# Optimization experiments

Hardware: AMD Instinct MI355X
Metric: run time of the kernel (lower is better)

## Reference

```python
import jax, jax.numpy as jnp
import numpy as np

SCALE_BASE = 512
EPS = 1e-5


def _xpos_factors(seq_len, head_dim):
    half = head_dim // 2
    # xpos scale vector: ((arange(0, hd, 2) + 0.4*hd) / (1.4*hd)) ** (pos / scale_base)
    s = (jnp.arange(0, head_dim, 2, dtype=jnp.float32) + 0.4 * head_dim) / (1.4 * head_dim)
    pos = jnp.arange(seq_len, dtype=jnp.float32)
    scale = s[None, :] ** (pos[:, None] / SCALE_BASE)          # (S, half)
    inv_freq = 1.0 / (10000.0 ** (jnp.arange(half, dtype=jnp.float32) / half))
    ang = pos[:, None] * inv_freq[None, :]                     # (S, half)
    return jnp.sin(ang), jnp.cos(ang), scale


def _dup_interleave(m):
    # (S, half) -> (S, head_dim): each column duplicated, interleaved
    return jnp.repeat(m, 2, axis=-1)


def _rotate_every_two(x):
    x1, x2 = x[..., ::2], x[..., 1::2]
    return jnp.stack((-x2, x1), axis=-1).reshape(x.shape)


def _apply_xpos(x, sin, cos, scale):
    sinf = _dup_interleave(sin * scale)                        # (S, hd)
    cosf = _dup_interleave(cos * scale)
    return x * cosf + _rotate_every_two(x) * sinf


def _decay_mask(gammas, seq_len, chunk_size):
    # D[h, i, j] = gamma_h ** |i - j| if j < ((i // chunk) + 1) * chunk else 0
    i = jnp.arange(seq_len)[:, None]
    j = jnp.arange(seq_len)[None, :]
    allowed = j < ((i // chunk_size) + 1) * chunk_size         # (S, S)
    expo = jnp.abs(i - j).astype(jnp.float32)
    D = gammas[:, None, None] ** expo[None]                    # (H, S, S)
    return jnp.where(allowed[None], D, 0.0)


def setup_inputs() -> dict:
    key = jax.random.key(0)
    B, S, hidden, H, hd, chunk = 4, 2048, 512, 8, 64, 64
    ks = jax.random.split(key, 6)
    return {
        "X": jax.random.normal(ks[0], (B, S, hidden), dtype=jnp.float32),
        "W_Q": jax.random.normal(ks[1], (H, hidden, hd), dtype=jnp.float32) / hidden,
        "W_K": jax.random.normal(ks[2], (H, hidden, hd), dtype=jnp.float32) / hidden,
        "W_V": jax.random.normal(ks[3], (H, hidden, hd), dtype=jnp.float32) / hidden,
        "W_G": jax.random.normal(ks[4], (hidden, H * hd), dtype=jnp.float32) / hidden,
        "W_O": jax.random.normal(ks[5], (H * hd, hidden), dtype=jnp.float32) / hidden,
        "gn_weight": jnp.ones((H * hd,), dtype=jnp.float32),
        "gn_bias": jnp.zeros((H * hd,), dtype=jnp.float32),
        "chunk_size": chunk,
    }


def reference(X, W_Q, W_K, W_V, W_G, W_O, gn_weight, gn_bias, chunk_size):
    B, S, hidden = X.shape
    H, _, hd = W_Q.shape
    # RetNet multi-scale decay rates
    gammas = 1.0 - jnp.exp(
        jnp.linspace(jnp.log(jnp.float32(1 / 32)), jnp.log(jnp.float32(1 / 512)), H)
    )
    D = _decay_mask(gammas, S, chunk_size)                     # (H, S, S)

    # per-head projections: n = heads
    Q = jnp.einsum("bsh,nhd->bnsd", X, W_Q)
    K = jnp.einsum("bsh,nhd->bnsd", X, W_K)
    V = jnp.einsum("bsh,nhd->bnsd", X, W_V)

    sin, cos, scale = _xpos_factors(S, hd)
    Q = _apply_xpos(Q, sin, cos, scale)                        # broadcast (S,hd) over (B,H,S,hd)
    K = _apply_xpos(K, sin, cos, 1.0 / scale)                  # downscale

    scores = jnp.einsum("bnsd,bntd->bnst", Q, K) * D[None]     # (B,H,S,S)
    Yh = jnp.einsum("bnst,bntd->bnsd", scores, V)              # (B,H,S,hd)

    # concat heads -> (B,S,H*hd), GroupNorm(heads) per token (stats over each head's hd channels)
    Y = Yh.transpose(0, 2, 1, 3)                               # (B,S,H,hd)
    mu = Y.mean(-1, keepdims=True)
    var = Y.var(-1, keepdims=True)
    Yn = (Y - mu) / jnp.sqrt(var + EPS)
    Yn = Yn.reshape(B, S, H * hd) * gn_weight + gn_bias

    gate = jax.nn.silu(X @ W_G)                                # swish(X W_G)
    return (gate * Yn) @ W_O
```

## Files before the change

kernel.cpp:

```cpp
#include <hip/hip_runtime.h>

#define B_   4
#define S_   2048
#define HID  512
#define H_   8
#define HD   64

typedef __attribute__((ext_vector_type(8))) short bf16x8;
typedef __attribute__((ext_vector_type(4))) float f32x4;

#define MFMA16(a, b, c) __builtin_amdgcn_mfma_f32_16x16x32_bf16(a, b, c, 0, 0, 0)

#define GAMMA_L0   (-3.4657359027997265f)
#define GAMMA_STEP (-0.3960841031771116f)

__device__ __forceinline__ void async16(const void* g, void* l) {
    __builtin_amdgcn_global_load_lds(
        (const __attribute__((address_space(1))) void*)g,
        (__attribute__((address_space(3))) void*)l, 16, 0, 0);
}

__device__ __forceinline__ unsigned short f2bf(float x) {
    unsigned u = __float_as_uint(x);
    return (unsigned short)((u + 0x7fffu + ((u >> 16) & 1u)) >> 16);
}
__device__ __forceinline__ float bfs2f(short s) {
    return __uint_as_float(((unsigned)(unsigned short)s) << 16);
}
__device__ __forceinline__ unsigned packbf(float lo, float hi) {
    return (unsigned)f2bf(lo) | ((unsigned)f2bf(hi) << 16);
}

__global__ __launch_bounds__(256) void prep(
    const float* __restrict__ X,
    const float* __restrict__ Wq, const float* __restrict__ Wk,
    const float* __restrict__ Wv, const float* __restrict__ Wg,
    const float* __restrict__ Wo,
    short* __restrict__ Xb,
    short* __restrict__ WqT, short* __restrict__ WkT, short* __restrict__ WvT,
    short* __restrict__ WgT, short* __restrict__ WoT,
    float4* __restrict__ Lut)
{
    __shared__ float T[64][65];
    const int bid = blockIdx.x, t = threadIdx.x;

    if (bid < 2048) {
        size_t i = ((size_t)bid * 256 + t) * 8;
        float4 a = *(const float4*)&X[i];
        float4 b = *(const float4*)&X[i + 4];
        union { int4 v; unsigned short s[8]; } u;
        u.s[0] = f2bf(a.x); u.s[1] = f2bf(a.y); u.s[2] = f2bf(a.z); u.s[3] = f2bf(a.w);
        u.s[4] = f2bf(b.x); u.s[5] = f2bf(b.y); u.s[6] = f2bf(b.z); u.s[7] = f2bf(b.w);
        *(int4*)&Xb[i] = u.v;
        return;
    }
    if (bid >= 2368) {
        int idx = (bid - 2368) * 256 + t;
        int s = idx >> 5, k = idx & 31;
        float invf = exp2f(-0.41524101186092035f * (float)k);
        float ang  = (float)s * invf;
        float sn = sinf(ang), cs = cosf(ang);
        float sk = ((float)(2 * k) + 25.6f) / 89.6f;
        float sc = exp2f(log2f(sk) * (float)s * (1.0f / 512.0f));
        Lut[idx] = (float4){cs * sc, sn * sc, cs / sc, sn / sc};
        return;
    }

    const int wb = bid - 2048;
    const float* ip; short* op; int ild;
    if (wb < 192) {
        int which = wb >> 6, rem = wb & 63, h = rem >> 3, kt = rem & 7;
        const float* src = which == 0 ? Wq : which == 1 ? Wk : Wv;
        short* dst       = which == 0 ? WqT : which == 1 ? WkT : WvT;
        ip = src + ((size_t)h * 512 + kt * 64) * 64;
        ild = 64;
        op = dst + (size_t)(h * 64) * 512 + kt * 64;
    } else {
        int rem = wb - 192, which = rem >> 6, r3 = rem & 63, nt = r3 >> 3, kt = r3 & 7;
        const float* src = which ? Wo : Wg;
        short* dst       = which ? WoT : WgT;
        ip = src + (size_t)(kt * 64) * 512 + nt * 64;
        ild = 512;
        op = dst + (size_t)(nt * 64) * 512 + kt * 64;
    }
    {
        int r = t >> 2, c0 = (t & 3) * 16;
        #pragma unroll
        for (int e = 0; e < 4; ++e) {
            float4 f = *(const float4*)&ip[(size_t)r * ild + c0 + e * 4];
            T[r][c0 + e*4 + 0] = f.x; T[r][c0 + e*4 + 1] = f.y;
            T[r][c0 + e*4 + 2] = f.z; T[r][c0 + e*4 + 3] = f.w;
        }
    }
    __syncthreads();
    {
        int cc = t >> 2, r0 = (t & 3) * 16;
        short* orow = op + (size_t)cc * 512;
        #pragma unroll
        for (int ii = 0; ii < 8; ++ii) {
            int lo = f2bf(T[r0 + 2*ii][cc]);
            int hi = f2bf(T[r0 + 2*ii + 1][cc]);
            *(int*)(orow + r0 + 2*ii) = (lo & 0xffff) | (hi << 16);
        }
    }
}

__device__ __forceinline__ void gemm_core64(const short* __restrict__ Ag,
                                            const short* __restrict__ Bg,
                                            short* As, short* Bs,
                                            f32x4 (&acc)[2][4])
{
    const int tid = threadIdx.x;
    const int L = tid & 63, quad = L >> 4, l16 = L & 15;
    const int w = tid >> 6;
    const int wrow = (w >> 1) * 32, wcol = (w & 1) * 64;

    for (int k0 = 0; k0 < 512; k0 += 32) {
        {
            int row = tid >> 2, c4 = (tid & 3) ^ (row & 3);
            async16(Ag + (size_t)row * 512 + k0 + c4 * 8, As + tid * 8);
        }
        #pragma unroll
        for (int j = 0; j < 2; ++j) {
            int idx = j * 256 + tid;
            int row = idx >> 2, c4 = (idx & 3) ^ (row & 3);
            async16(Bg + (size_t)row * 512 + k0 + c4 * 8, Bs + idx * 8);
        }
        __syncthreads();

        bf16x8 af[2], bfr[4];
        #pragma unroll
        for (int a = 0; a < 2; ++a) {
            int m = wrow + a * 16 + l16;
            af[a] = *(const bf16x8*)&As[m * 32 + (quad ^ (m & 3)) * 8];
        }
        #pragma unroll
        for (int b = 0; b < 4; ++b) {
            int n = wcol + b * 16 + l16;
            bfr[b] = *(const bf16x8*)&Bs[n * 32 + (quad ^ (n & 3)) * 8];
        }
        #pragma unroll
        for (int a = 0; a < 2; ++a)
            #pragma unroll
            for (int b = 0; b < 4; ++b)
                acc[a][b] = MFMA16(af[a], bfr[b], acc[a][b]);
        __syncthreads();
    }
}

__global__ __launch_bounds__(256) void fused_gemm(
    const short* __restrict__ Xb, const short* __restrict__ WT,
    const float4* __restrict__ Lut,
    short* __restrict__ Qb, short* __restrict__ Kb, short* __restrict__ Vb,
    short* __restrict__ Gb)
{
    __shared__ short SM[64 * 136];
    f32x4 acc[2][4];
    #pragma unroll
    for (int a = 0; a < 2; ++a)
        #pragma unroll
        for (int b = 0; b < 4; ++b) acc[a][b] = (f32x4){0.f, 0.f, 0.f, 0.f};

    gemm_core64(Xb + (size_t)blockIdx.y * 64 * 512,
                WT + (size_t)blockIdx.x * 128 * 512, SM, SM + 2048, acc);

    const int tid = threadIdx.x, L = tid & 63, quad = L >> 4, l16 = L & 15;
    const int w = tid >> 6, wrow = (w >> 1) * 32, wcol = (w & 1) * 64;
    const int zone = blockIdx.x >> 2;
    short* Out = (zone == 0) ? Qb : (zone == 1) ? Kb : Vb;

    #pragma unroll
    for (int b = 0; b < 4; ++b) {
        int ncol = (blockIdx.x & 3) * 128 + wcol + b * 16 + l16;
        int d = ncol & 63, k = d >> 1;
        int colE = wcol + b * 16 + (l16 & ~1);
        #pragma unroll
        for (int a = 0; a < 2; ++a) {
            #pragma unroll
            for (int r = 0; r < 4; ++r) {
                int m = blockIdx.y * 64 + wrow + a * 16 + quad * 4 + r;
                int s = m & 2047;
                float v = acc[a][b][r];
                unsigned word;
                if (zone == 3) {
                    float g = v / (1.0f + __expf(-v));
                    float part = __shfl_xor(g, 1);
                    word = packbf(g, part);
                } else {
                    float part = __shfl_xor(v, 1);
                    float e = (d & 1) ? part : v;
                    float o = (d & 1) ? v : part;
                    if (zone == 2) {
                        word = packbf(e, o);
                    } else {
                        float4 f = Lut[s * 32 + k];
                        float cs = (zone == 0) ? f.x : f.z;
                        float sn = (zone == 0) ? f.y : f.w;
                        word = packbf(e * cs - o * sn, o * cs + e * sn);
                    }
                }
                if (!(l16 & 1))
                    *(int*)&SM[(wrow + a * 16 + quad * 4 + r) * 136 + colE] = word;
            }
        }
    }
    __syncthreads();
    #pragma unroll
    for (int j = 0; j < 4; ++j) {
        int idx = j * 256 + tid;
        int row = idx >> 4, c0 = (idx & 15) * 8;
        int m = blockIdx.y * 64 + row;
        int n = (blockIdx.x & 3) * 128 + c0;
        if (zone == 3) {
            *(int4*)&Gb[(size_t)m * 512 + n] = *(const int4*)&SM[row * 136 + c0];
        } else {
            int bb = m >> 11, s = m & 2047;
            int h = n >> 6, d = n & 63;
            *(int4*)&Out[(((size_t)bb * 8 + h) * 2048 + s) * 64 + d] =
                *(const int4*)&SM[row * 136 + c0];
        }
    }
}

__global__ __launch_bounds__(256) void out_gemm(
    const short* __restrict__ Zb, const short* __restrict__ WoT,
    float* __restrict__ Of)
{
    __shared__ short SM[6144];
    f32x4 acc[2][4];
    #pragma unroll
    for (int a = 0; a < 2; ++a)
        #pragma unroll
        for (int b = 0; b < 4; ++b) acc[a][b] = (f32x4){0.f, 0.f, 0.f, 0.f};

    gemm_core64(Zb + (size_t)blockIdx.y * 64 * 512,
                WoT + (size_t)blockIdx.x * 128 * 512, SM, SM + 2048, acc);

    const int tid = threadIdx.x, L = tid & 63, quad = L >> 4, l16 = L & 15;
    const int w = tid >> 6, wrow = (w >> 1) * 32, wcol = (w & 1) * 64;
    #pragma unroll
    for (int b = 0; b < 4; ++b) {
        int ncol = blockIdx.x * 128 + wcol + b * 16 + l16;
        #pragma unroll
        for (int a = 0; a < 2; ++a)
            #pragma unroll
            for (int r = 0; r < 4; ++r) {
                int m = blockIdx.y * 64 + wrow + a * 16 + quad * 4 + r;
                Of[(size_t)m * 512 + ncol] = acc[a][b][r];
            }
    }
}

__global__ __launch_bounds__(256) void ret_g(
    const short* __restrict__ Kb, const short* __restrict__ Vb,
    short* __restrict__ Gt)
{
    __shared__ short Kt[64 * 72];
    __shared__ short Vt[64 * 72];
    const int tid = threadIdx.x, L = tid & 63, quad = L >> 4, l16 = L & 15;
    const int w = tid >> 6;
    const int c = blockIdx.x, bn = blockIdx.y, hh = bn & 7;

    float gamma = 1.0f - expf(GAMMA_L0 + GAMMA_STEP * (float)hh);
    float lg = log2f(gamma);

    {
        const short* kg = Kb + ((size_t)bn * 2048 + c * 64 + L) * 64 + w * 16;
        const short* vg = Vb + ((size_t)bn * 2048 + c * 64 + L) * 64 + w * 16;
        float wgt = exp2f(lg * (float)(64 - L));
        int4 k0 = *(const int4*)kg; int4 k1 = *(const int4*)(kg + 8);
        int4 v0 = *(const int4*)vg; int4 v1 = *(const int4*)(vg + 8);
        short* kt = Kt + L; short* vt = Vt + L;
        #pragma unroll
        for (int q = 0; q < 4; ++q) {
            int uk = ((const int*)&k0)[q];
            kt[(w*16 + 2*q)     * 72] = (short)f2bf(bfs2f((short)uk) * wgt);
            kt[(w*16 + 2*q + 1) * 72] = (short)f2bf(bfs2f((short)(uk >> 16)) * wgt);
            int uv = ((const int*)&v0)[q];
            vt[(w*16 + 2*q)     * 72] = (short)uv;
            vt[(w*16 + 2*q + 1) * 72] = (short)(uv >> 16);
        }
        #pragma unroll
        for (int q = 0; q < 4; ++q) {
            int uk = ((const int*)&k1)[q];
            kt[(w*16 + 8 + 2*q) * 72] = (short)f2bf(bfs2f((short)uk) * wgt);
            kt[(w*16 + 9 + 2*q) * 72] = (short)f2bf(bfs2f((short)(uk >> 16)) * wgt);
            int uv = ((const int*)&v1)[q];
            vt[(w*16 + 8 + 2*q) * 72] = (short)uv;
            vt[(w*16 + 9 + 2*q) * 72] = (short)(uv >> 16);
        }
    }
    __syncthreads();

    bf16x8 a0 = *(const bf16x8*)&Vt[(w * 16 + l16) * 72 + quad * 8];
    bf16x8 a1 = *(const bf16x8*)&Vt[(w * 16 + l16) * 72 + 32 + quad * 8];
    short* Gp = Gt + ((size_t)bn * 32 + c) * 4096;
    #pragma unroll
    for (int b = 0; b < 4; ++b) {
        bf16x8 b0 = *(const bf16x8*)&Kt[(b * 16 + l16) * 72 + quad * 8];
        bf16x8 b1 = *(const bf16x8*)&Kt[(b * 16 + l16) * 72 + 32 + quad * 8];
        f32x4 acc = (f32x4){0.f, 0.f, 0.f, 0.f};
        acc = MFMA16(a0, b0, acc);
        acc = MFMA16(a1, b1, acc);
        #pragma unroll
        for (int r = 0; r < 4; ++r) {
            float v = acc[r];
            float part = __shfl_xor(v, 1);
            unsigned word = packbf(v, part);
            if (!(l16 & 1))
                *(int*)&Gp[(w*16 + quad*4 + r) * 64 + b * 16 + (l16 & ~1)] = word;
        }
    }
}

__global__ __launch_bounds__(256) void ret_scan(short* __restrict__ GM)
{
    const int tid = threadIdx.x, seg = blockIdx.x, bn = blockIdx.y, hh = bn & 7;
    float gamma = 1.0f - expf(GAMMA_L0 + GAMMA_STEP * (float)hh);
    float g64 = exp2f(log2f(gamma) * 64.0f);

    size_t base = (size_t)bn * 32 * 4096 + seg * 1024 + tid * 4;
    float m0 = 0.f, m1 = 0.f, m2 = 0.f, m3 = 0.f;
    #pragma unroll 4
    for (int c = 0; c < 32; ++c) {
        int2* p = (int2*)&GM[base + (size_t)c * 4096];
        int2 g = *p;
        *p = make_int2((int)packbf(m0, m1), (int)packbf(m2, m3));
        m0 = g64 * m0 + bfs2f((short)g.x);
        m1 = g64 * m1 + bfs2f((short)(g.x >> 16));
        m2 = g64 * m2 + bfs2f((short)g.y);
        m3 = g64 * m3 + bfs2f((short)(g.y >> 16));
    }
}

__global__ __launch_bounds__(256) void ret_main(
    const short* __restrict__ Qb, const short* __restrict__ Kb,
    const short* __restrict__ Vb, const short* __restrict__ Mb,
    short* __restrict__ Yb)
{
    __shared__ short Qs[4096];
    __shared__ short Ks[4096];
    __shared__ short Ms[4096];
    __shared__ short Vt[64 * 72];
    __shared__ short Pw[4][16 * 72];

    const int tid = threadIdx.x, L = tid & 63, quad = L >> 4, l16 = L & 15;
    const int w = tid >> 6;
    const int c = blockIdx.x, bn = blockIdx.y, hh = bn & 7, bb = bn >> 3;

    float gamma = 1.0f - expf(GAMMA_L0 + GAMMA_STEP * (float)hh);
    float lg = log2f(gamma);

    float Dabs[4][4];
    #pragma unroll
    for (int b = 0; b < 4; ++b)
        #pragma unroll
        for (int r = 0; r < 4; ++r) {
            int dlt = (w * 16 + quad * 4 + r) - (b * 16 + l16);
            Dabs[b][r] = exp2f(lg * fabsf((float)dlt));
        }
    float gq[4];
    #pragma unroll
    for (int r = 0; r < 4; ++r)
        gq[r] = exp2f(lg * (float)(w * 16 + quad * 4 + r));

    {
        const short* qg = Qb + ((size_t)bn * 2048 + c * 64 + w * 16 + (L >> 2)) * 64 + (L & 3) * 8;
        async16(qg,      Qs + w * 512 + L * 8);
        async16(qg + 32, Qs + 2048 + w * 512 + L * 8);
        const short* kg = Kb + ((size_t)bn * 2048 + c * 64 + w * 16 + (L >> 2)) * 64 + (L & 3) * 8;
        async16(kg,      Ks + w * 512 + L * 8);
        async16(kg + 32, Ks + 2048 + w * 512 + L * 8);
        const short* mg = Mb + ((size_t)bn * 32 + c) * 4096 + (w * 16 + (L >> 2)) * 64 + (L & 3) * 8;
        async16(mg,      Ms + w * 512 + L * 8);
        async16(mg + 32, Ms + 2048 + w * 512 + L * 8);
    }
    {
        const short* vg = Vb + ((size_t)bn * 2048 + c * 64 + L) * 64 + w * 16;
        int4 v0 = *(const int4*)vg;
        int4 v1 = *(const int4*)(vg + 8);
        short* vt = Vt + L;
        #pragma unroll
        for (int q = 0; q < 4; ++q) {
            int u = ((const int*)&v0)[q];
            vt[(w*16 + 2*q)     * 72] = (short)u;
            vt[(w*16 + 2*q + 1) * 72] = (short)(u >> 16);
        }
        #pragma unroll
        for (int q = 0; q < 4; ++q) {
            int u = ((const int*)&v1)[q];
            vt[(w*16 + 8 + 2*q) * 72] = (short)u;
            vt[(w*16 + 9 + 2*q) * 72] = (short)(u >> 16);
        }
    }
    __syncthreads();

    bf16x8 aQ0 = *(const bf16x8*)&Qs[(w * 16 + l16) * 32 + quad * 8];
    bf16x8 aQ1 = *(const bf16x8*)&Qs[2048 + (w * 16 + l16) * 32 + quad * 8];
    f32x4 accM[4];
    #pragma unroll
    for (int b = 0; b < 4; ++b) {
        bf16x8 k0 = *(const bf16x8*)&Ks[(b * 16 + l16) * 32 + quad * 8];
        bf16x8 k1 = *(const bf16x8*)&Ks[2048 + (b * 16 + l16) * 32 + quad * 8];
        f32x4 S = (f32x4){0.f, 0.f, 0.f, 0.f};
        S = MFMA16(aQ0, k0, S);
        S = MFMA16(aQ1, k1, S);
        #pragma unroll
        for (int r = 0; r < 4; ++r)
            Pw[w][(quad * 4 + r) * 72 + b * 16 + l16] = (short)f2bf(S[r] * Dabs[b][r]);

        bf16x8 m0 = *(const bf16x8*)&Ms[(b * 16 + l16) * 32 + quad * 8];
        bf16x8 m1 = *(const bf16x8*)&Ms[2048 + (b * 16 + l16) * 32 + quad * 8];
        f32x4 Mv = (f32x4){0.f, 0.f, 0.f, 0.f};
        Mv = MFMA16(aQ0, m0, Mv);
        Mv = MFMA16(aQ1, m1, Mv);
        accM[b] = Mv;
    }

    bf16x8 aP0 = *(const bf16x8*)&Pw[w][l16 * 72 + quad * 8];
    bf16x8 aP1 = *(const bf16x8*)&Pw[w][l16 * 72 + 32 + quad * 8];
    #pragma unroll
    for (int b2 = 0; b2 < 4; ++b2) {
        bf16x8 v0f = *(const bf16x8*)&Vt[(b2 * 16 + l16) * 72 + quad * 8];
        bf16x8 v1f = *(const bf16x8*)&Vt[(b2 * 16 + l16) * 72 + 32 + quad * 8];
        f32x4 y = accM[b2];
        f32x4 yv = (f32x4){0.f, 0.f, 0.f, 0.f};
        yv = MFMA16(aP0, v0f, yv);
        yv = MFMA16(aP1, v1f, yv);
        #pragma unroll
        for (int r = 0; r < 4; ++r) {
            float yy = yv[r] + gq[r] * y[r];
            float part = __shfl_xor(yy, 1);
            unsigned word = packbf(yy, part);
            if (!(l16 & 1)) {
                int il = w * 16 + quad * 4 + r;
                int d = b2 * 16 + (l16 & ~1);
                *(int*)&Yb[(((size_t)bb * 2048 + c * 64 + il) * 8 + hh) * 64 + d] = word;
            }
        }
    }
}

__global__ __launch_bounds__(256) void gn_kernel(
    const short* __restrict__ Yb, const short* __restrict__ Gb,
    const float* __restrict__ gw, const float* __restrict__ gb,
    short* __restrict__ Zb)
{
    const int t = threadIdx.x, w = t >> 6, L = t & 63;
    const int unit = blockIdx.x * 4 + w;
    const size_t idx = (size_t)unit * 64 + L;

    float y = bfs2f(Yb[idx]);
    float sum = y, sq = y * y;
    #pragma unroll
    for (int off = 32; off; off >>= 1) {
        sum += __shfl_xor(sum, off);
        sq  += __shfl_xor(sq, off);
    }
    float mu  = sum * (1.0f / 64.0f);
    float var = sq * (1.0f / 64.0f) - mu * mu;
    float rstd = rsqrtf(var + 1e-5f);

    int j = (unit & 7) * 64 + L;
    float yn = (y - mu) * rstd * gw[j] + gb[j];
    Zb[idx] = (short)f2bf(bfs2f(Gb[idx]) * yn);
}

extern "C" void kernel_launch(void* const* d_in, const int* in_sizes, int n_in,
                              void* d_out, int out_size, void* d_ws, size_t ws_size,
                              hipStream_t stream)
{
    const float* X  = (const float*)d_in[0];
    const float* Wq = (const float*)d_in[1];
    const float* Wk = (const float*)d_in[2];
    const float* Wv = (const float*)d_in[3];
    const float* Wg = (const float*)d_in[4];
    const float* Wo = (const float*)d_in[5];
    const float* gw = (const float*)d_in[6];
    const float* gb = (const float*)d_in[7];

    char* ws = (char*)d_ws;
    short* Xb  = (short*)ws;
    short* WqT = (short*)(ws + 8388608);
    short* WkT = WqT + 262144;
    short* WvT = WkT + 262144;
    short* WgT = WvT + 262144;
    short* WoT = WgT + 262144;
    short* Qb  = (short*)(ws + 11010048);
    short* Kb  = Qb + 4194304;
    short* Vb  = Kb + 4194304;
    float4* Lut = (float4*)(ws + 36175872);
    short* GM  = (short*)(ws + 37224448);
    short* Yb  = (short*)(ws + 45613056);
    short* Gb  = (short*)(ws + 54001664);
    short* Zb  = Vb;

    prep<<<2624, 256, 0, stream>>>(X, Wq, Wk, Wv, Wg, Wo,
                                   Xb, WqT, WkT, WvT, WgT, WoT, Lut);
    fused_gemm<<<dim3(16, 128), 256, 0, stream>>>(Xb, WqT, Lut, Qb, Kb, Vb, Gb);
    ret_g<<<dim3(32, 32), 256, 0, stream>>>(Kb, Vb, GM);
    ret_scan<<<dim3(4, 32), 256, 0, stream>>>(GM);
    ret_main<<<dim3(32, 32), 256, 0, stream>>>(Qb, Kb, Vb, GM, Yb);
    gn_kernel<<<16384, 256, 0, stream>>>(Yb, Gb, gw, gb, Zb);
    out_gemm<<<dim3(4, 128), 256, 0, stream>>>(Zb, WoT, (float*)d_out);
}
```

Baseline: 183.9 us.

## Double-buffer GEMM K loop and fuse GroupNorm+gate into retention kernel

The shared GEMM core now double-buffers its LDS tiles so the async load of the next K slice overlaps the MFMAs on the current one, with one barrier per iteration and a changed XOR swizzle. GroupNorm statistics, affine transform and the silu-gate multiply move into the epilogue of ret_main using in-wave shuffles, which removes the gn_kernel launch and the round trip of Y through global memory. Costs are twice the LDS per GEMM block, which may lower occupancy, and a heavier ret_main epilogue with scattered Gb reads.

```diff
diff --git a/kernel.cpp b/kernel.cpp
--- a/kernel.cpp
+++ b/kernel.cpp
@@ -105,47 +105,60 @@
     }
 }
 
+__device__ __forceinline__ void stage64(const short* __restrict__ Ag,
+                                        const short* __restrict__ Bg,
+                                        int k0, short* As, short* Bs, int tid)
+{
+    {
+        int row = tid >> 2, c4 = (tid & 3) ^ ((row >> 1) & 3);
+        async16(Ag + (size_t)row * 512 + k0 + c4 * 8, As + tid * 8);
+    }
+    #pragma unroll
+    for (int j = 0; j < 2; ++j) {
+        int idx = j * 256 + tid;
+        int row = idx >> 2, c4 = (idx & 3) ^ ((row >> 1) & 3);
+        async16(Bg + (size_t)row * 512 + k0 + c4 * 8, Bs + idx * 8);
+    }
+}
+
 __device__ __forceinline__ void gemm_core64(const short* __restrict__ Ag,
                                             const short* __restrict__ Bg,
-                                            short* As, short* Bs,
-                                            f32x4 (&acc)[2][4])
+                                            short* SM, f32x4 (&acc)[2][4])
 {
     const int tid = threadIdx.x;
     const int L = tid & 63, quad = L >> 4, l16 = L & 15;
     const int w = tid >> 6;
     const int wrow = (w >> 1) * 32, wcol = (w & 1) * 64;
 
-    for (int k0 = 0; k0 < 512; k0 += 32) {
-        {
-            int row = tid >> 2, c4 = (tid & 3) ^ (row & 3);
-            async16(Ag + (size_t)row * 512 + k0 + c4 * 8, As + tid * 8);
-        }
-        #pragma unroll
-        for (int j = 0; j < 2; ++j) {
-            int idx = j * 256 + tid;
-            int row = idx >> 2, c4 = (idx & 3) ^ (row & 3);
-            async16(Bg + (size_t)row * 512 + k0 + c4 * 8, Bs + idx * 8);
-        }
+    stage64(Ag, Bg, 0, SM, SM + 2048, tid);
+    #pragma unroll
+    for (int it = 0; it < 16; ++it) {
+        const int cur = (it & 1) * 6144;
         __syncthreads();
-
+        if (it + 1 < 16) {
+            const int nxt = ((it + 1) & 1) * 6144;
+            stage64(Ag, Bg, (it + 1) * 32, SM + nxt, SM + nxt + 2048, tid);
+        }
+        const short* as = SM + cur;
+        const short* bs = SM + cur + 2048;
         bf16x8 af[2], bfr[4];
         #pragma unroll
         for (int a = 0; a < 2; ++a) {
             int m = wrow + a * 16 + l16;
-            af[a] = *(const bf16x8*)&As[m * 32 + (quad ^ (m & 3)) * 8];
+            af[a] = *(const bf16x8*)&as[m * 32 + (quad ^ ((m >> 1) & 3)) * 8];
         }
         #pragma unroll
         for (int b = 0; b < 4; ++b) {
             int n = wcol + b * 16 + l16;
-            bfr[b] = *(const bf16x8*)&Bs[n * 32 + (quad ^ (n & 3)) * 8];
+            bfr[b] = *(const bf16x8*)&bs[n * 32 + (quad ^ ((n >> 1) & 3)) * 8];
         }
         #pragma unroll
         for (int a = 0; a < 2; ++a)
             #pragma unroll
             for (int b = 0; b < 4; ++b)
                 acc[a][b] = MFMA16(af[a], bfr[b], acc[a][b]);
-        __syncthreads();
-    }
+    }
+    __syncthreads();
 }
 
 __global__ __launch_bounds__(256) void fused_gemm(
@@ -154,7 +167,7 @@
     short* __restrict__ Qb, short* __restrict__ Kb, short* __restrict__ Vb,
     short* __restrict__ Gb)
 {
-    __shared__ short SM[64 * 136];
+    __shared__ short SM[12288];
     f32x4 acc[2][4];
     #pragma unroll
     for (int a = 0; a < 2; ++a)
@@ -162,7 +175,7 @@
         for (int b = 0; b < 4; ++b) acc[a][b] = (f32x4){0.f, 0.f, 0.f, 0.f};
 
     gemm_core64(Xb + (size_t)blockIdx.y * 64 * 512,
-                WT + (size_t)blockIdx.x * 128 * 512, SM, SM + 2048, acc);
+                WT + (size_t)blockIdx.x * 128 * 512, SM, acc);
 
     const int tid = threadIdx.x, L = tid & 63, quad = L >> 4, l16 = L & 15;
     const int w = tid >> 6, wrow = (w >> 1) * 32, wcol = (w & 1) * 64;
@@ -226,7 +239,7 @@
     const short* __restrict__ Zb, const short* __restrict__ WoT,
     float* __restrict__ Of)
 {
-    __shared__ short SM[6144];
+    __shared__ short SM[12288];
     f32x4 acc[2][4];
     #pragma unroll
     for (int a = 0; a < 2; ++a)
@@ -234,7 +247,7 @@
         for (int b = 0; b < 4; ++b) acc[a][b] = (f32x4){0.f, 0.f, 0.f, 0.f};
 
     gemm_core64(Zb + (size_t)blockIdx.y * 64 * 512,
-                WoT + (size_t)blockIdx.x * 128 * 512, SM, SM + 2048, acc);
+                WoT + (size_t)blockIdx.x * 128 * 512, SM, acc);
 
     const int tid = threadIdx.x, L = tid & 63, quad = L >> 4, l16 = L & 15;
     const int w = tid >> 6, wrow = (w >> 1) * 32, wcol = (w & 1) * 64;
@@ -336,7 +349,9 @@
 __global__ __launch_bounds__(256) void ret_main(
     const short* __restrict__ Qb, const short* __restrict__ Kb,
     const short* __restrict__ Vb, const short* __restrict__ Mb,
-    short* __restrict__ Yb)
+    const short* __restrict__ Gb,
+    const float* __restrict__ gw, const float* __restrict__ gb,
+    short* __restrict__ Zb)
 {
     __shared__ short Qs[4096];
     __shared__ short Ks[4096];
@@ -419,51 +434,48 @@
 
     bf16x8 aP0 = *(const bf16x8*)&Pw[w][l16 * 72 + quad * 8];
     bf16x8 aP1 = *(const bf16x8*)&Pw[w][l16 * 72 + 32 + quad * 8];
+    f32x4 Y4[4];
     #pragma unroll
     for (int b2 = 0; b2 < 4; ++b2) {
         bf16x8 v0f = *(const bf16x8*)&Vt[(b2 * 16 + l16) * 72 + quad * 8];
         bf16x8 v1f = *(const bf16x8*)&Vt[(b2 * 16 + l16) * 72 + 32 + quad * 8];
-        f32x4 y = accM[b2];
         f32x4 yv = (f32x4){0.f, 0.f, 0.f, 0.f};
         yv = MFMA16(aP0, v0f, yv);
         yv = MFMA16(aP1, v1f, yv);
         #pragma unroll
-        for (int r = 0; r < 4; ++r) {
-            float yy = yv[r] + gq[r] * y[r];
-            float part = __shfl_xor(yy, 1);
-            unsigned word = packbf(yy, part);
-            if (!(l16 & 1)) {
-                int il = w * 16 + quad * 4 + r;
-                int d = b2 * 16 + (l16 & ~1);
-                *(int*)&Yb[(((size_t)bb * 2048 + c * 64 + il) * 8 + hh) * 64 + d] = word;
-            }
-        }
-    }
-}
-
-__global__ __launch_bounds__(256) void gn_kernel(
-    const short* __restrict__ Yb, const short* __restrict__ Gb,
-    const float* __restrict__ gw, const float* __restrict__ gb,
-    short* __restrict__ Zb)
-{
-    const int t = threadIdx.x, w = t >> 6, L = t & 63;
-    const int unit = blockIdx.x * 4 + w;
-    const size_t idx = (size_t)unit * 64 + L;
-
-    float y = bfs2f(Yb[idx]);
-    float sum = y, sq = y * y;
-    #pragma unroll
-    for (int off = 32; off; off >>= 1) {
-        sum += __shfl_xor(sum, off);
-        sq  += __shfl_xor(sq, off);
-    }
-    float mu  = sum * (1.0f / 64.0f);
-    float var = sq * (1.0f / 64.0f) - mu * mu;
-    float rstd = rsqrtf(var + 1e-5f);
-
-    int j = (unit & 7) * 64 + L;
-    float yn = (y - mu) * rstd * gw[j] + gb[j];
-    Zb[idx] = (short)f2bf(bfs2f(Gb[idx]) * yn);
+        for (int r = 0; r < 4; ++r)
+            Y4[b2][r] = yv[r] + gq[r] * accM[b2][r];
+    }
+
+    #pragma unroll
+    for (int r = 0; r < 4; ++r) {
+        float s1 = 0.f, s2 = 0.f;
+        #pragma unroll
+        for (int b2 = 0; b2 < 4; ++b2) {
+            float v = Y4[b2][r];
+            s1 += v; s2 += v * v;
+        }
+        #pragma unroll
+        for (int off = 1; off < 16; off <<= 1) {
+            s1 += __shfl_xor(s1, off);
+            s2 += __shfl_xor(s2, off);
+        }
+        float mu = s1 * (1.0f / 64.0f);
+        float var = s2 * (1.0f / 64.0f) - mu * mu;
+        float rstd = rsqrtf(var + 1e-5f);
+
+        int il = w * 16 + quad * 4 + r;
+        size_t row = (size_t)bb * 2048 + c * 64 + il;
+        #pragma unroll
+        for (int b2 = 0; b2 < 4; ++b2) {
+            int j = hh * 64 + b2 * 16 + l16;
+            float yn = (Y4[b2][r] - mu) * rstd * gw[j] + gb[j];
+            float z = bfs2f(Gb[row * 512 + j]) * yn;
+            float part = __shfl_xor(z, 1);
+            if (!(l16 & 1))
+                *(int*)&Zb[row * 512 + hh * 64 + b2 * 16 + (l16 & ~1)] = packbf(z, part);
+        }
+    }
 }
 
 extern "C" void kernel_launch(void* const* d_in, const int* in_sizes, int n_in,
@@ -491,16 +503,14 @@
     short* Vb  = Kb + 4194304;
     float4* Lut = (float4*)(ws + 36175872);
     short* GM  = (short*)(ws + 37224448);
-    short* Yb  = (short*)(ws + 45613056);
+    short* Zb  = (short*)(ws + 45613056);
     short* Gb  = (short*)(ws + 54001664);
-    short* Zb  = Vb;
 
     prep<<<2624, 256, 0, stream>>>(X, Wq, Wk, Wv, Wg, Wo,
                                    Xb, WqT, WkT, WvT, WgT, WoT, Lut);
     fused_gemm<<<dim3(16, 128), 256, 0, stream>>>(Xb, WqT, Lut, Qb, Kb, Vb, Gb);
     ret_g<<<dim3(32, 32), 256, 0, stream>>>(Kb, Vb, GM);
     ret_scan<<<dim3(4, 32), 256, 0, stream>>>(GM);
-    ret_main<<<dim3(32, 32), 256, 0, stream>>>(Qb, Kb, Vb, GM, Yb);
-    gn_kernel<<<16384, 256, 0, stream>>>(Yb, Gb, gw, gb, Zb);
+    ret_main<<<dim3(32, 32), 256, 0, stream>>>(Qb, Kb, Vb, GM, Gb, gw, gb, Zb);
     out_gemm<<<dim3(4, 128), 256, 0, stream>>>(Zb, WoT, (float*)d_out);
 }
```

Result: faster. 180.2 us (-2.0%).
